# Kernel tuning notes

Hardware: AMD Instinct MI355X
Metric: run time of the kernel (lower is better)

Reference implementation:

```python
import jax, jax.numpy as jnp
import numpy as np

E, D, O, G, H, K = 8, 1024, 1024, 512, 2048, 2
B = 8192

def _xavier(key, shape):
    fan_in, fan_out = shape[-2], shape[-1]
    lim = float(np.sqrt(6.0 / (fan_in + fan_out)))
    return jax.random.uniform(key, shape, jnp.float32, -lim, lim)

def setup_inputs() -> dict:
    key = jax.random.key(0)
    ks = jax.random.split(key, 6)
    x = jax.random.normal(ks[0], (B, D), jnp.float32)
    # stacked expert params (xavier-uniform weights, zero bias like torch init)
    W1 = _xavier(ks[1], (E, D, H))
    b1 = jnp.zeros((E, H), jnp.float32)
    W2 = _xavier(ks[2], (E, H, O))
    b2 = jnp.zeros((E, O), jnp.float32)
    # gate params
    Wg1 = _xavier(ks[3], (D, G))
    bg1 = jnp.zeros((G,), jnp.float32)
    Wg2 = _xavier(ks[4], (G, E))
    bg2 = jnp.zeros((E,), jnp.float32)
    return {"x": x, "W1": W1, "b1": b1, "W2": W2, "b2": b2,
            "Wg1": Wg1, "bg1": bg1, "Wg2": Wg2, "bg2": bg2}

def reference(x, W1, b1, W2, b2, Wg1, bg1, Wg2, bg2):
    batch = x.shape[0]
    # gate (dropout inactive in eval)
    gate_logits = jax.nn.relu(x @ Wg1 + bg1) @ Wg2 + bg2          # [B,E]
    gate_scores = jax.nn.softmax(gate_logits, axis=1)
    top_k_scores, top_k_indices = jax.lax.top_k(gate_scores, K)   # [B,K]
    # dense all-expert MLP (mirrors torch.stack over experts)
    h = jax.nn.relu(jnp.einsum('bd,edh->ebh', x, W1) + b1[:, None, :])   # [E,B,H]
    expert_outputs = jnp.einsum('ebh,eho->beo', h, W2) + b2[None, :, :]  # [B,E,O]
    # gather top-k expert outputs, scale, combine
    selected = jnp.take_along_axis(expert_outputs, top_k_indices[:, :, None], axis=1)  # [B,K,O]
    scaled = selected * top_k_scores[:, :, None]
    scaled = scaled / (jnp.sum(top_k_scores, axis=1, keepdims=True)[:, :, None] + 1e-9)
    combined = jnp.sum(scaled, axis=1)                            # [B,O]
    # auxiliary loss
    one_hot = jax.nn.one_hot(top_k_indices, E, dtype=jnp.float32) # [B,K,E]
    expert_load = jnp.sum(one_hot, axis=(0, 1)) / (batch + 1e-9)
    load_balancing_loss = jnp.var(expert_load, ddof=1)            # torch var is unbiased
    entropy = -jnp.mean(jnp.sum(gate_scores * jnp.log(gate_scores + 1e-9), axis=1))
    aux_loss = load_balancing_loss + entropy
    return combined, aux_loss
```

## Files before the change

kernel.cpp:

```cpp
#include <hip/hip_runtime.h>

#define B_ 8192
#define D_ 1024
#define O_ 1024
#define G_ 512
#define H_ 2048
#define E_ 8
#define ROWSP (B_ * 2 + E_ * 128)
#define TAU 0.01f

typedef unsigned short u16;
using f32x4  = __attribute__((ext_vector_type(4))) float;
using s16x8  = __attribute__((ext_vector_type(8))) short;

__device__ __forceinline__ u16 f2bf(float f) {
  union { float f; unsigned u; } v; v.f = f;
  unsigned r = v.u + 0x7FFFu + ((v.u >> 16) & 1u);
  return (u16)(r >> 16);
}
__device__ __forceinline__ float bf2f(u16 h) {
  union { unsigned u; float f; } v; v.u = ((unsigned)h) << 16; return v.f;
}
__device__ __forceinline__ void gload16(const void* g, void* l) {
  __builtin_amdgcn_global_load_lds(
      (const __attribute__((address_space(1))) unsigned int*)g,
      (__attribute__((address_space(3))) unsigned int*)l, 16, 0, 0);
}
__device__ __forceinline__ int xcd_swz(int bid, int nwg) {
  return (bid & 7) * (nwg >> 3) + (bid >> 3);
}
__device__ __forceinline__ int stage_kc(int t) {
  return (((t & 3) ^ ((t >> 3) & 3)) * 8);
}
__device__ __forceinline__ int frag_idx(int lane, int i) {
  int row = i * 16 + (lane & 15);
  int s = (lane >> 4) ^ ((lane >> 1) & 3);
  return (row * 4 + s) * 8;
}

#define PREP_CAST_BLK (B_ * D_ / 4 / 256)
#define PREP_WG1_BLK  ((G_ / 32) * (D_ / 32))
#define PREP_W1_BLK   ((H_ / 32) * (D_ / 32) * E_)
#define PREP_W2_BLK   ((O_ / 32) * (H_ / 32) * E_)

__device__ __forceinline__ void tr_cast_tile(const float* __restrict__ src,
                                             u16* __restrict__ dhi,
                                             u16* __restrict__ dlo,
                                             int R, int C, int bx, int by,
                                             float (*tile)[33], int t) {
  int c0 = bx * 32, r0 = by * 32;
  {
    int row = t >> 3, col4 = (t & 7) * 4;
    float4 v = *(const float4*)(src + (size_t)(r0 + row) * C + c0 + col4);
    tile[row][col4] = v.x; tile[row][col4 + 1] = v.y;
    tile[row][col4 + 2] = v.z; tile[row][col4 + 3] = v.w;
  }
  __syncthreads();
  {
    int c = t >> 3, r4 = (t & 7) * 4;
    float v0 = tile[r4 + 0][c], v1 = tile[r4 + 1][c];
    float v2 = tile[r4 + 2][c], v3 = tile[r4 + 3][c];
    ushort4 hi;
    hi.x = f2bf(v0); hi.y = f2bf(v1); hi.z = f2bf(v2); hi.w = f2bf(v3);
    *(ushort4*)(dhi + (size_t)(c0 + c) * R + r0 + r4) = hi;
    if (dlo) {
      ushort4 lo;
      lo.x = f2bf(v0 - bf2f(hi.x)); lo.y = f2bf(v1 - bf2f(hi.y));
      lo.z = f2bf(v2 - bf2f(hi.z)); lo.w = f2bf(v3 - bf2f(hi.w));
      *(ushort4*)(dlo + (size_t)(c0 + c) * R + r0 + r4) = lo;
    }
  }
}

__global__ __launch_bounds__(256) void k_prep(const float* __restrict__ x,
                                              u16* __restrict__ xhi, u16* __restrict__ xlo,
                                              const float* __restrict__ Wg1,
                                              u16* __restrict__ wg1h, u16* __restrict__ wg1l,
                                              const float* __restrict__ W1, u16* __restrict__ w1t,
                                              const float* __restrict__ W2, u16* __restrict__ w2t) {
  __shared__ float tile[32][33];
  int t = threadIdx.x;
  int b = blockIdx.x;
  if (b < PREP_CAST_BLK) {
    int i = b * 256 + t;
    float4 v = ((const float4*)x)[i];
    u16 h0 = f2bf(v.x), h1 = f2bf(v.y), h2 = f2bf(v.z), h3 = f2bf(v.w);
    ushort4 hi; hi.x = h0; hi.y = h1; hi.z = h2; hi.w = h3;
    ushort4 lo;
    lo.x = f2bf(v.x - bf2f(h0)); lo.y = f2bf(v.y - bf2f(h1));
    lo.z = f2bf(v.z - bf2f(h2)); lo.w = f2bf(v.w - bf2f(h3));
    ((ushort4*)xhi)[i] = hi; ((ushort4*)xlo)[i] = lo;
    return;
  }
  b -= PREP_CAST_BLK;
  if (b < PREP_WG1_BLK) {
    tr_cast_tile(Wg1, wg1h, wg1l, D_, G_, b & 15, b >> 4, tile, t);
    return;
  }
  b -= PREP_WG1_BLK;
  if (b < PREP_W1_BLK) {
    int e = b >> 11, rr = b & 2047;
    size_t ofs = (size_t)e * D_ * H_;
    tr_cast_tile(W1 + ofs, w1t + ofs, nullptr, D_, H_, rr & 63, rr >> 6, tile, t);
    return;
  }
  b -= PREP_W1_BLK;
  {
    int e = b >> 11, rr = b & 2047;
    size_t ofs = (size_t)e * H_ * O_;
    tr_cast_tile(W2 + ofs, w2t + ofs, nullptr, H_, O_, rr & 31, rr >> 5, tile, t);
  }
}

__global__ __launch_bounds__(256) void k_gate_gemm1(const u16* __restrict__ xhi,
                                                    const u16* __restrict__ xlo,
                                                    const u16* __restrict__ whi,
                                                    const u16* __restrict__ wlo,
                                                    const float* __restrict__ bg1,
                                                    float* __restrict__ G1) {
  __shared__ u16 Ah[2048], Al[2048], Bh[4096], Bl[4096];
  int work = xcd_swz(blockIdx.x, (G_ / 128) * (B_ / 64));
  int m0 = (work >> 2) * 64, n0 = (work & 3) * 128;
  int t = threadIdx.x;
  int wave = t >> 6, lane = t & 63;
  int wm = wave >> 1, wn = wave & 1;

  const f32x4 z = {0.f, 0.f, 0.f, 0.f};
  f32x4 acc[2][4];
#pragma unroll
  for (int i = 0; i < 2; ++i)
#pragma unroll
    for (int j = 0; j < 4; ++j) acc[i][j] = z;

  int ar = t >> 2, ac = stage_kc(t);
  const u16* xh0 = xhi + (size_t)(m0 + ar) * D_ + ac;
  const u16* xl0 = xlo + (size_t)(m0 + ar) * D_ + ac;
  const u16* wh0 = whi + (size_t)(n0 + ar) * D_ + ac;
  const u16* wh1 = whi + (size_t)(n0 + 64 + ar) * D_ + ac;
  const u16* wl0 = wlo + (size_t)(n0 + ar) * D_ + ac;
  const u16* wl1 = wlo + (size_t)(n0 + 64 + ar) * D_ + ac;

  for (int k0 = 0; k0 < D_; k0 += 32) {
    gload16(xh0 + k0, &Ah[t * 8]);
    gload16(xl0 + k0, &Al[t * 8]);
    gload16(wh0 + k0, &Bh[t * 8]); gload16(wh1 + k0, &Bh[2048 + t * 8]);
    gload16(wl0 + k0, &Bl[t * 8]); gload16(wl1 + k0, &Bl[2048 + t * 8]);
    __syncthreads();
    s16x8 ah[2], al[2], bh[4], bl[4];
#pragma unroll
    for (int i = 0; i < 2; ++i) {
      ah[i] = *(const s16x8*)&Ah[frag_idx(lane, wm * 2 + i)];
      al[i] = *(const s16x8*)&Al[frag_idx(lane, wm * 2 + i)];
    }
#pragma unroll
    for (int j = 0; j < 4; ++j) {
      bh[j] = *(const s16x8*)&Bh[wn * 2048 + frag_idx(lane, j)];
      bl[j] = *(const s16x8*)&Bl[wn * 2048 + frag_idx(lane, j)];
    }
#pragma unroll
    for (int i = 0; i < 2; ++i)
#pragma unroll
      for (int j = 0; j < 4; ++j) {
        acc[i][j] = __builtin_amdgcn_mfma_f32_16x16x32_bf16(ah[i], bh[j], acc[i][j], 0, 0, 0);
        acc[i][j] = __builtin_amdgcn_mfma_f32_16x16x32_bf16(ah[i], bl[j], acc[i][j], 0, 0, 0);
        acc[i][j] = __builtin_amdgcn_mfma_f32_16x16x32_bf16(al[i], bh[j], acc[i][j], 0, 0, 0);
      }
    __syncthreads();
  }
#pragma unroll
  for (int j = 0; j < 4; ++j) {
    int col = n0 + wn * 64 + j * 16 + (lane & 15);
    float bias = bg1[col];
#pragma unroll
    for (int i = 0; i < 2; ++i)
#pragma unroll
      for (int q = 0; q < 4; ++q) {
        int row = m0 + wm * 32 + i * 16 + (lane >> 4) * 4 + q;
        float v = acc[i][j][q] + bias;
        G1[(size_t)row * G_ + col] = v > 0.f ? v : 0.f;
      }
  }
}

__global__ __launch_bounds__(256) void k_gate_logits(const float* __restrict__ G1,
                                                     const float* __restrict__ Wg2,
                                                     const float* __restrict__ bg2,
                                                     float* __restrict__ logits,
                                                     int* __restrict__ flaglist,
                                                     int* __restrict__ nflag) {
  int t = threadIdx.x, wave = t >> 6, lane = t & 63;
  int row = blockIdx.x * 4 + wave;

  float4 g0 = *(const float4*)(G1 + (size_t)row * G_ + lane * 8);
  float4 g1 = *(const float4*)(G1 + (size_t)row * G_ + lane * 8 + 4);
  float g[8] = {g0.x, g0.y, g0.z, g0.w, g1.x, g1.y, g1.z, g1.w};
  float p[8] = {0, 0, 0, 0, 0, 0, 0, 0};
#pragma unroll
  for (int cc = 0; cc < 8; ++cc) {
    int c = lane * 8 + cc;
    float4 w0 = *(const float4*)(Wg2 + c * 8);
    float4 w1 = *(const float4*)(Wg2 + c * 8 + 4);
    p[0] += g[cc] * w0.x; p[1] += g[cc] * w0.y; p[2] += g[cc] * w0.z; p[3] += g[cc] * w0.w;
    p[4] += g[cc] * w1.x; p[5] += g[cc] * w1.y; p[6] += g[cc] * w1.z; p[7] += g[cc] * w1.w;
  }
#pragma unroll
  for (int off = 32; off >= 1; off >>= 1)
#pragma unroll
    for (int e = 0; e < 8; ++e) p[e] += __shfl_xor(p[e], off);
  if (lane == 0) {
    float l1 = -1e30f, l2 = -1e30f, l3 = -1e30f;
#pragma unroll
    for (int e = 0; e < 8; ++e) {
      float v = p[e] + bg2[e];
      logits[(size_t)row * 8 + e] = v;
      if (v > l1) { l3 = l2; l2 = l1; l1 = v; }
      else if (v > l2) { l3 = l2; l2 = v; }
      else if (v > l3) { l3 = v; }
    }
    if (l2 - l3 < TAU) {
      int pos = atomicAdd(nflag, 1);
      flaglist[pos] = row;
    }
  }
}

__global__ __launch_bounds__(256) void k_gate_fixup(const float* __restrict__ x,
                                                    const float* __restrict__ Wg1,
                                                    const float* __restrict__ bg1,
                                                    const float* __restrict__ Wg2,
                                                    const float* __restrict__ bg2,
                                                    const int* __restrict__ flaglist,
                                                    const int* __restrict__ nflag,
                                                    float* __restrict__ logits) {
  __shared__ float xs[1024];
  __shared__ float red[256][9];
  int t = threadIdx.x;
  int n = *nflag;
  for (int i = blockIdx.x; i < n; i += gridDim.x) {
    int row = flaglist[i];
    ((float4*)xs)[t] = ((const float4*)(x + (size_t)row * D_))[t];
    __syncthreads();
    int c0 = t * 2;
    float h0 = 0.f, h1 = 0.f;
#pragma unroll 8
    for (int d = 0; d < D_; ++d) {
      float xv = xs[d];
      float2 w = *(const float2*)(Wg1 + (size_t)d * G_ + c0);
      h0 += xv * w.x; h1 += xv * w.y;
    }
    h0 += bg1[c0]; h1 += bg1[c0 + 1];
    h0 = h0 > 0.f ? h0 : 0.f; h1 = h1 > 0.f ? h1 : 0.f;
#pragma unroll
    for (int e = 0; e < 8; ++e)
      red[t][e] = h0 * Wg2[c0 * 8 + e] + h1 * Wg2[(c0 + 1) * 8 + e];
    __syncthreads();
    for (int s = 128; s >= 1; s >>= 1) {
      if (t < s) {
#pragma unroll
        for (int e = 0; e < 8; ++e) red[t][e] += red[t + s][e];
      }
      __syncthreads();
    }
    if (t < 8) logits[(size_t)row * 8 + t] = red[0][t] + bg2[t];
    __syncthreads();
  }
}

__global__ __launch_bounds__(256) void k_gate_final(const float* __restrict__ logits,
                                                    int* __restrict__ topidx,
                                                    float* __restrict__ wnorm,
                                                    int* __restrict__ counts,
                                                    float* __restrict__ entacc) {
  __shared__ int cnt_s[8];
  __shared__ float ent_s[4];
  int t = threadIdx.x;
  if (t < 8) cnt_s[t] = 0;
  __syncthreads();
  int row = blockIdx.x * 256 + t;
  float4 a = ((const float4*)logits)[(size_t)row * 2];
  float4 b = ((const float4*)logits)[(size_t)row * 2 + 1];
  float L[8] = {a.x, a.y, a.z, a.w, b.x, b.y, b.z, b.w};
  float m = L[0];
#pragma unroll
  for (int e = 1; e < 8; ++e) m = fmaxf(m, L[e]);
  float s[8], Z = 0.f;
#pragma unroll
  for (int e = 0; e < 8; ++e) { s[e] = expf(L[e] - m); Z += s[e]; }
  float inv = 1.f / Z;
  float sc[8];
#pragma unroll
  for (int e = 0; e < 8; ++e) sc[e] = s[e] * inv;
  int i1 = 0;
#pragma unroll
  for (int e = 1; e < 8; ++e) if (L[e] > L[i1]) i1 = e;
  int i2 = (i1 == 0) ? 1 : 0;
#pragma unroll
  for (int e = 0; e < 8; ++e) if (e != i1 && L[e] > L[i2]) i2 = e;
  float s1 = sc[i1], s2 = sc[i2];
  float denom = s1 + s2 + 1e-9f;
  topidx[row * 2] = i1; topidx[row * 2 + 1] = i2;
  wnorm[row * 2] = s1 / denom; wnorm[row * 2 + 1] = s2 / denom;
  atomicAdd(&cnt_s[i1], 1); atomicAdd(&cnt_s[i2], 1);
  float ent = 0.f;
#pragma unroll
  for (int e = 0; e < 8; ++e) ent -= sc[e] * logf(sc[e] + 1e-9f);
#pragma unroll
  for (int off = 32; off >= 1; off >>= 1) ent += __shfl_xor(ent, off);
  if ((t & 63) == 0) ent_s[t >> 6] = ent;
  __syncthreads();
  if (t == 0) atomicAdd(entacc, ent_s[0] + ent_s[1] + ent_s[2] + ent_s[3]);
  if (t < 8) atomicAdd(&counts[t], cnt_s[t]);
}

__global__ void k_scan(const int* __restrict__ counts, const float* __restrict__ entacc,
                       int* __restrict__ aoff, float* __restrict__ aux_out) {
  if (threadIdx.x == 0 && blockIdx.x == 0) {
    int off = 0; aoff[0] = 0;
    float ld[8]; float mean = 0.f;
    for (int e = 0; e < 8; ++e) {
      ld[e] = (float)counts[e] / (8192.0f + 1e-9f);
      mean += ld[e];
      off += ((counts[e] + 127) >> 7) << 7;
      aoff[e + 1] = off;
    }
    mean *= 0.125f;
    float var = 0.f;
    for (int e = 0; e < 8; ++e) { float d = ld[e] - mean; var += d * d; }
    var *= (1.0f / 7.0f);
    *aux_out = var + entacc[0] / 8192.0f;
  }
}

__global__ __launch_bounds__(256) void k_scatter(const int* __restrict__ topidx,
                                                 const float* __restrict__ wnorm,
                                                 const int* __restrict__ aoff,
                                                 int* __restrict__ fill,
                                                 int* __restrict__ tok_list,
                                                 float* __restrict__ wroute,
                                                 int* __restrict__ pos_of) {
  int t = blockIdx.x * 256 + threadIdx.x;
  if (t >= B_ * 2) return;
  int e = topidx[t];
  int pos = aoff[e] + atomicAdd(&fill[e], 1);
  tok_list[pos] = t >> 1;
  wroute[pos] = wnorm[t];
  pos_of[t] = pos;
}


__global__ __launch_bounds__(256) void k_egemm1(const u16* __restrict__ xhi,
                                                const u16* __restrict__ w1t,
                                                const float* __restrict__ b1v,
                                                const int* __restrict__ tok_list,
                                                const int* __restrict__ aoff,
                                                u16* __restrict__ hbuf) {
  __shared__ u16 As[2][4096], Bs[2][4096];
  int work = xcd_swz(blockIdx.x, (H_ / 128) * (ROWSP / 128));
  int rt = work >> 4;
  int n0 = (work & 15) * 128;
  int row0 = rt * 128;
  if (row0 >= aoff[8]) return;
  int e = 0;
  while (row0 >= aoff[e + 1]) ++e;
  int t = threadIdx.x, wave = t >> 6, lane = t & 63;
  int wm = wave >> 1, wn = wave & 1;
  const u16* w1e = w1t + (size_t)e * H_ * D_;

  int ar = t >> 2, ac = stage_kc(t);
  int tok0 = tok_list[row0 + ar];       if ((unsigned)tok0 >= B_) tok0 = 0;
  int tok1 = tok_list[row0 + 64 + ar];  if ((unsigned)tok1 >= B_) tok1 = 0;
  const u16* a0 = xhi + (size_t)tok0 * D_ + ac;
  const u16* a1 = xhi + (size_t)tok1 * D_ + ac;
  const u16* bb0 = w1e + (size_t)(n0 + ar) * D_ + ac;
  const u16* bb1 = w1e + (size_t)(n0 + 64 + ar) * D_ + ac;

  const f32x4 z = {0.f, 0.f, 0.f, 0.f};
  f32x4 acc[4][4];
#pragma unroll
  for (int i = 0; i < 4; ++i)
#pragma unroll
    for (int j = 0; j < 4; ++j) acc[i][j] = z;

  gload16(a0, &As[0][t * 8]);  gload16(a1, &As[0][2048 + t * 8]);
  gload16(bb0, &Bs[0][t * 8]); gload16(bb1, &Bs[0][2048 + t * 8]);
  __syncthreads();

  const int NT = D_ / 32;
  for (int kt = 0; kt < NT; ++kt) {
    int cur = kt & 1, nxt = cur ^ 1;
    if (kt + 1 < NT) {
      int kk = (kt + 1) * 32;
      gload16(a0 + kk, &As[nxt][t * 8]);  gload16(a1 + kk, &As[nxt][2048 + t * 8]);
      gload16(bb0 + kk, &Bs[nxt][t * 8]); gload16(bb1 + kk, &Bs[nxt][2048 + t * 8]);
    }
    s16x8 af[4], bf[4];
#pragma unroll
    for (int i = 0; i < 4; ++i) {
      af[i] = *(const s16x8*)&As[cur][wm * 2048 + frag_idx(lane, i)];
      bf[i] = *(const s16x8*)&Bs[cur][wn * 2048 + frag_idx(lane, i)];
    }
#pragma unroll
    for (int i = 0; i < 4; ++i)
#pragma unroll
      for (int j = 0; j < 4; ++j)
        acc[i][j] = __builtin_amdgcn_mfma_f32_16x16x32_bf16(af[i], bf[j], acc[i][j], 0, 0, 0);
    __syncthreads();
  }
#pragma unroll
  for (int j = 0; j < 4; ++j) {
    int col = n0 + wn * 64 + j * 16 + (lane & 15);
    float bias = b1v[e * H_ + col];
#pragma unroll
    for (int i = 0; i < 4; ++i)
#pragma unroll
      for (int q = 0; q < 4; ++q) {
        int row = row0 + wm * 64 + i * 16 + (lane >> 4) * 4 + q;
        float v = acc[i][j][q] + bias;
        hbuf[(size_t)row * H_ + col] = f2bf(v > 0.f ? v : 0.f);
      }
  }
}

__global__ __launch_bounds__(256) void k_egemm2(const u16* __restrict__ hbuf,
                                                const u16* __restrict__ w2t,
                                                const float* __restrict__ b2v,
                                                const int* __restrict__ aoff,
                                                const float* __restrict__ wroute,
                                                u16* __restrict__ rbuf) {
  __shared__ u16 As[2][4096], Bs[2][4096];
  int work = xcd_swz(blockIdx.x, (O_ / 128) * (ROWSP / 128));
  int rt = work >> 3;
  int n0 = (work & 7) * 128;
  int row0 = rt * 128;
  if (row0 >= aoff[8]) return;
  int e = 0;
  while (row0 >= aoff[e + 1]) ++e;
  int t = threadIdx.x, wave = t >> 6, lane = t & 63;
  int wm = wave >> 1, wn = wave & 1;
  const u16* w2e = w2t + (size_t)e * O_ * H_;

  int ar = t >> 2, ac = stage_kc(t);
  const u16* a0 = hbuf + (size_t)(row0 + ar) * H_ + ac;
  const u16* a1 = hbuf + (size_t)(row0 + 64 + ar) * H_ + ac;
  const u16* bb0 = w2e + (size_t)(n0 + ar) * H_ + ac;
  const u16* bb1 = w2e + (size_t)(n0 + 64 + ar) * H_ + ac;

  const f32x4 z = {0.f, 0.f, 0.f, 0.f};
  f32x4 acc[4][4];
#pragma unroll
  for (int i = 0; i < 4; ++i)
#pragma unroll
    for (int j = 0; j < 4; ++j) acc[i][j] = z;

  gload16(a0, &As[0][t * 8]);  gload16(a1, &As[0][2048 + t * 8]);
  gload16(bb0, &Bs[0][t * 8]); gload16(bb1, &Bs[0][2048 + t * 8]);
  __syncthreads();

  const int NT = H_ / 32;
  for (int kt = 0; kt < NT; ++kt) {
    int cur = kt & 1, nxt = cur ^ 1;
    if (kt + 1 < NT) {
      int kk = (kt + 1) * 32;
      gload16(a0 + kk, &As[nxt][t * 8]);  gload16(a1 + kk, &As[nxt][2048 + t * 8]);
      gload16(bb0 + kk, &Bs[nxt][t * 8]); gload16(bb1 + kk, &Bs[nxt][2048 + t * 8]);
    }
    s16x8 af[4], bf[4];
#pragma unroll
    for (int i = 0; i < 4; ++i) {
      af[i] = *(const s16x8*)&As[cur][wm * 2048 + frag_idx(lane, i)];
      bf[i] = *(const s16x8*)&Bs[cur][wn * 2048 + frag_idx(lane, i)];
    }
#pragma unroll
    for (int i = 0; i < 4; ++i)
#pragma unroll
      for (int j = 0; j < 4; ++j)
        acc[i][j] = __builtin_amdgcn_mfma_f32_16x16x32_bf16(af[i], bf[j], acc[i][j], 0, 0, 0);
    __syncthreads();
  }
#pragma unroll
  for (int i = 0; i < 4; ++i)
#pragma unroll
    for (int q = 0; q < 4; ++q) {
      int row = row0 + wm * 64 + i * 16 + (lane >> 4) * 4 + q;
      float wv = wroute[row];
#pragma unroll
      for (int j = 0; j < 4; ++j) {
        int col = n0 + wn * 64 + j * 16 + (lane & 15);
        float bias = b2v[e * O_ + col];
        rbuf[(size_t)row * O_ + col] = f2bf((acc[i][j][q] + bias) * wv);
      }
    }
}

__global__ __launch_bounds__(256) void k_combine(const u16* __restrict__ rbuf,
                                                 const int* __restrict__ pos_of,
                                                 float* __restrict__ out) {
  int t = threadIdx.x;
  int tok = blockIdx.x * 2 + (t >> 7);
  int c = (t & 127) * 8;
  int p0 = pos_of[tok * 2], p1 = pos_of[tok * 2 + 1];
  const u16* r0 = rbuf + (size_t)p0 * O_ + c;
  const u16* r1 = rbuf + (size_t)p1 * O_ + c;
  ushort4 a0 = *(const ushort4*)r0, a1 = *(const ushort4*)(r0 + 4);
  ushort4 b0 = *(const ushort4*)r1, b1 = *(const ushort4*)(r1 + 4);
  float4 o0, o1;
  o0.x = bf2f(a0.x) + bf2f(b0.x); o0.y = bf2f(a0.y) + bf2f(b0.y);
  o0.z = bf2f(a0.z) + bf2f(b0.z); o0.w = bf2f(a0.w) + bf2f(b0.w);
  o1.x = bf2f(a1.x) + bf2f(b1.x); o1.y = bf2f(a1.y) + bf2f(b1.y);
  o1.z = bf2f(a1.z) + bf2f(b1.z); o1.w = bf2f(a1.w) + bf2f(b1.w);
  float* op = out + (size_t)tok * O_ + c;
  *(float4*)op = o0; *(float4*)(op + 4) = o1;
}

static const size_t o_xhi  = 0;
static const size_t o_xlo  = o_xhi + (size_t)B_ * D_ * 2;
static const size_t o_w1t  = o_xlo + (size_t)B_ * D_ * 2;
static const size_t o_w2t  = o_w1t + (size_t)E_ * H_ * D_ * 2;
static const size_t o_wg1h = o_w2t + (size_t)E_ * O_ * H_ * 2;
static const size_t o_wg1l = o_wg1h + (size_t)G_ * D_ * 2;
static const size_t o_G1   = o_wg1l + (size_t)G_ * D_ * 2;
static const size_t o_h    = o_G1 + (size_t)B_ * G_ * 4;
static const size_t o_idx  = o_h + (size_t)ROWSP * H_ * 2;
static const size_t o_wn   = o_idx + (size_t)B_ * 2 * 4;
static const size_t o_pos  = o_wn + (size_t)B_ * 2 * 4;
static const size_t o_tok  = o_pos + (size_t)B_ * 2 * 4;
static const size_t o_wr   = o_tok + (size_t)ROWSP * 4;
static const size_t o_cnt  = o_wr + (size_t)ROWSP * 4;
static const size_t o_fill = o_cnt + 32;
static const size_t o_ent  = o_cnt + 64;
static const size_t o_nfl  = o_cnt + 96;
static const size_t o_aoff = o_cnt + 128;
static const size_t o_logits = o_cnt + 256;
static const size_t o_flag   = o_logits + (size_t)B_ * 8 * 4;
static const size_t o_rbuf = o_xlo;

extern "C" void kernel_launch(void* const* d_in, const int* in_sizes, int n_in,
                              void* d_out, int out_size, void* d_ws, size_t ws_size,
                              hipStream_t stream) {
  const float* x   = (const float*)d_in[0];
  const float* W1  = (const float*)d_in[1];
  const float* b1  = (const float*)d_in[2];
  const float* W2  = (const float*)d_in[3];
  const float* b2  = (const float*)d_in[4];
  const float* Wg1 = (const float*)d_in[5];
  const float* bg1 = (const float*)d_in[6];
  const float* Wg2 = (const float*)d_in[7];
  const float* bg2 = (const float*)d_in[8];
  float* out = (float*)d_out;
  char* ws = (char*)d_ws;

  u16* xhi  = (u16*)(ws + o_xhi);
  u16* xlo  = (u16*)(ws + o_xlo);
  u16* w1t  = (u16*)(ws + o_w1t);
  u16* w2t  = (u16*)(ws + o_w2t);
  u16* wg1h = (u16*)(ws + o_wg1h);
  u16* wg1l = (u16*)(ws + o_wg1l);
  float* G1 = (float*)(ws + o_G1);
  u16* hbuf = (u16*)(ws + o_h);
  int* topidx = (int*)(ws + o_idx);
  float* wnorm = (float*)(ws + o_wn);
  int* pos_of = (int*)(ws + o_pos);
  int* tok_list = (int*)(ws + o_tok);
  float* wroute = (float*)(ws + o_wr);
  int* counts = (int*)(ws + o_cnt);
  int* fill = (int*)(ws + o_fill);
  float* entacc = (float*)(ws + o_ent);
  int* nflag = (int*)(ws + o_nfl);
  int* aoff = (int*)(ws + o_aoff);
  float* logits = (float*)(ws + o_logits);
  int* flaglist = (int*)(ws + o_flag);
  u16* rbuf = (u16*)(ws + o_rbuf);

  hipMemsetAsync(ws + o_cnt, 0, 128, stream);

  k_prep<<<PREP_CAST_BLK + PREP_WG1_BLK + PREP_W1_BLK + PREP_W2_BLK, 256, 0, stream>>>(
      x, xhi, xlo, Wg1, wg1h, wg1l, W1, w1t, W2, w2t);

  k_gate_gemm1<<<(G_ / 128) * (B_ / 64), 256, 0, stream>>>(xhi, xlo, wg1h, wg1l, bg1, G1);
  k_gate_logits<<<B_ / 4, 256, 0, stream>>>(G1, Wg2, bg2, logits, flaglist, nflag);
  k_gate_fixup<<<128, 256, 0, stream>>>(x, Wg1, bg1, Wg2, bg2, flaglist, nflag, logits);
  k_gate_final<<<B_ / 256, 256, 0, stream>>>(logits, topidx, wnorm, counts, entacc);
  k_scan<<<1, 64, 0, stream>>>(counts, entacc, aoff, out + (size_t)B_ * O_);
  k_scatter<<<(B_ * 2) / 256, 256, 0, stream>>>(topidx, wnorm, aoff, fill, tok_list, wroute, pos_of);

  k_egemm1<<<(H_ / 128) * (ROWSP / 128), 256, 0, stream>>>(xhi, w1t, b1, tok_list, aoff, hbuf);
  k_egemm2<<<(O_ / 128) * (ROWSP / 128), 256, 0, stream>>>(hbuf, w2t, b2, aoff, wroute, rbuf);
  k_combine<<<B_ / 2, 256, 0, stream>>>(rbuf, pos_of, out);
}
```

Before: 496.9 us.

## Fuse gate fixup, scan and scatter into gate kernels; drop x low-part split

Removes the low bf16 residual of x, so the gate GEMM does two MFMAs per tile instead of three and the prep kernel writes half as much x data. To make up for the lost precision, TAU is raised so more rows with close second and third logits are recomputed in fp32. That recomputation now runs inside k_gate_logits, per block, instead of in a separate fixup kernel. k_scan and k_scatter are folded into k_gate_final through a grid-wide spin barrier on an arrival counter, and the memset is replaced by zeroing inside k_prep. The spin barrier assumes all 32 blocks of k_gate_final are resident at once, and the in-block fixup can serialize blocks that hold flagged rows.

```diff
diff --git a/kernel.cpp b/kernel.cpp
--- a/kernel.cpp
+++ b/kernel.cpp
@@ -7,7 +7,7 @@
 #define H_ 2048
 #define E_ 8
 #define ROWSP (B_ * 2 + E_ * 128)
-#define TAU 0.01f
+#define TAU 0.04f
 
 typedef unsigned short u16;
 using f32x4  = __attribute__((ext_vector_type(4))) float;
@@ -73,23 +73,22 @@
 }
 
 __global__ __launch_bounds__(256) void k_prep(const float* __restrict__ x,
-                                              u16* __restrict__ xhi, u16* __restrict__ xlo,
+                                              u16* __restrict__ xhi,
                                               const float* __restrict__ Wg1,
                                               u16* __restrict__ wg1h, u16* __restrict__ wg1l,
                                               const float* __restrict__ W1, u16* __restrict__ w1t,
-                                              const float* __restrict__ W2, u16* __restrict__ w2t) {
+                                              const float* __restrict__ W2, u16* __restrict__ w2t,
+                                              int* __restrict__ zeroarea) {
   __shared__ float tile[32][33];
   int t = threadIdx.x;
   int b = blockIdx.x;
   if (b < PREP_CAST_BLK) {
+    if (b == 0 && t < 32) zeroarea[t] = 0;
     int i = b * 256 + t;
     float4 v = ((const float4*)x)[i];
-    u16 h0 = f2bf(v.x), h1 = f2bf(v.y), h2 = f2bf(v.z), h3 = f2bf(v.w);
-    ushort4 hi; hi.x = h0; hi.y = h1; hi.z = h2; hi.w = h3;
-    ushort4 lo;
-    lo.x = f2bf(v.x - bf2f(h0)); lo.y = f2bf(v.y - bf2f(h1));
-    lo.z = f2bf(v.z - bf2f(h2)); lo.w = f2bf(v.w - bf2f(h3));
-    ((ushort4*)xhi)[i] = hi; ((ushort4*)xlo)[i] = lo;
+    ushort4 hi;
+    hi.x = f2bf(v.x); hi.y = f2bf(v.y); hi.z = f2bf(v.z); hi.w = f2bf(v.w);
+    ((ushort4*)xhi)[i] = hi;
     return;
   }
   b -= PREP_CAST_BLK;
@@ -113,12 +112,11 @@
 }
 
 __global__ __launch_bounds__(256) void k_gate_gemm1(const u16* __restrict__ xhi,
-                                                    const u16* __restrict__ xlo,
                                                     const u16* __restrict__ whi,
                                                     const u16* __restrict__ wlo,
                                                     const float* __restrict__ bg1,
                                                     float* __restrict__ G1) {
-  __shared__ u16 Ah[2048], Al[2048], Bh[4096], Bl[4096];
+  __shared__ u16 Ah[2048], Bh[4096], Bl[4096];
   int work = xcd_swz(blockIdx.x, (G_ / 128) * (B_ / 64));
   int m0 = (work >> 2) * 64, n0 = (work & 3) * 128;
   int t = threadIdx.x;
@@ -134,7 +132,6 @@
 
   int ar = t >> 2, ac = stage_kc(t);
   const u16* xh0 = xhi + (size_t)(m0 + ar) * D_ + ac;
-  const u16* xl0 = xlo + (size_t)(m0 + ar) * D_ + ac;
   const u16* wh0 = whi + (size_t)(n0 + ar) * D_ + ac;
   const u16* wh1 = whi + (size_t)(n0 + 64 + ar) * D_ + ac;
   const u16* wl0 = wlo + (size_t)(n0 + ar) * D_ + ac;
@@ -142,16 +139,13 @@
 
   for (int k0 = 0; k0 < D_; k0 += 32) {
     gload16(xh0 + k0, &Ah[t * 8]);
-    gload16(xl0 + k0, &Al[t * 8]);
     gload16(wh0 + k0, &Bh[t * 8]); gload16(wh1 + k0, &Bh[2048 + t * 8]);
     gload16(wl0 + k0, &Bl[t * 8]); gload16(wl1 + k0, &Bl[2048 + t * 8]);
     __syncthreads();
-    s16x8 ah[2], al[2], bh[4], bl[4];
-#pragma unroll
-    for (int i = 0; i < 2; ++i) {
+    s16x8 ah[2], bh[4], bl[4];
+#pragma unroll
+    for (int i = 0; i < 2; ++i)
       ah[i] = *(const s16x8*)&Ah[frag_idx(lane, wm * 2 + i)];
-      al[i] = *(const s16x8*)&Al[frag_idx(lane, wm * 2 + i)];
-    }
 #pragma unroll
     for (int j = 0; j < 4; ++j) {
       bh[j] = *(const s16x8*)&Bh[wn * 2048 + frag_idx(lane, j)];
@@ -163,7 +157,6 @@
       for (int j = 0; j < 4; ++j) {
         acc[i][j] = __builtin_amdgcn_mfma_f32_16x16x32_bf16(ah[i], bh[j], acc[i][j], 0, 0, 0);
         acc[i][j] = __builtin_amdgcn_mfma_f32_16x16x32_bf16(ah[i], bl[j], acc[i][j], 0, 0, 0);
-        acc[i][j] = __builtin_amdgcn_mfma_f32_16x16x32_bf16(al[i], bh[j], acc[i][j], 0, 0, 0);
       }
     __syncthreads();
   }
@@ -183,11 +176,15 @@
 }
 
 __global__ __launch_bounds__(256) void k_gate_logits(const float* __restrict__ G1,
+                                                     const float* __restrict__ x,
+                                                     const float* __restrict__ Wg1,
+                                                     const float* __restrict__ bg1,
                                                      const float* __restrict__ Wg2,
                                                      const float* __restrict__ bg2,
-                                                     float* __restrict__ logits,
-                                                     int* __restrict__ flaglist,
-                                                     int* __restrict__ nflag) {
+                                                     float* __restrict__ logits) {
+  __shared__ int flagsm[4];
+  __shared__ float xs[1024];
+  __shared__ float red[256][9];
   int t = threadIdx.x, wave = t >> 6, lane = t & 63;
   int row = blockIdx.x * 4 + wave;
 
@@ -217,52 +214,38 @@
       else if (v > l2) { l3 = l2; l2 = v; }
       else if (v > l3) { l3 = v; }
     }
-    if (l2 - l3 < TAU) {
-      int pos = atomicAdd(nflag, 1);
-      flaglist[pos] = row;
-    }
-  }
-}
-
-__global__ __launch_bounds__(256) void k_gate_fixup(const float* __restrict__ x,
-                                                    const float* __restrict__ Wg1,
-                                                    const float* __restrict__ bg1,
-                                                    const float* __restrict__ Wg2,
-                                                    const float* __restrict__ bg2,
-                                                    const int* __restrict__ flaglist,
-                                                    const int* __restrict__ nflag,
-                                                    float* __restrict__ logits) {
-  __shared__ float xs[1024];
-  __shared__ float red[256][9];
-  int t = threadIdx.x;
-  int n = *nflag;
-  for (int i = blockIdx.x; i < n; i += gridDim.x) {
-    int row = flaglist[i];
-    ((float4*)xs)[t] = ((const float4*)(x + (size_t)row * D_))[t];
-    __syncthreads();
-    int c0 = t * 2;
-    float h0 = 0.f, h1 = 0.f;
+    flagsm[wave] = (l2 - l3 < TAU) ? 1 : 0;
+  }
+  __syncthreads();
+  for (int r = 0; r < 4; ++r) {
+    if (flagsm[r]) {
+      int rr = blockIdx.x * 4 + r;
+      ((float4*)xs)[t] = ((const float4*)(x + (size_t)rr * D_))[t];
+      __syncthreads();
+      int c0 = t * 2;
+      float h0 = 0.f, h1 = 0.f;
 #pragma unroll 8
-    for (int d = 0; d < D_; ++d) {
-      float xv = xs[d];
-      float2 w = *(const float2*)(Wg1 + (size_t)d * G_ + c0);
-      h0 += xv * w.x; h1 += xv * w.y;
-    }
-    h0 += bg1[c0]; h1 += bg1[c0 + 1];
-    h0 = h0 > 0.f ? h0 : 0.f; h1 = h1 > 0.f ? h1 : 0.f;
-#pragma unroll
-    for (int e = 0; e < 8; ++e)
-      red[t][e] = h0 * Wg2[c0 * 8 + e] + h1 * Wg2[(c0 + 1) * 8 + e];
-    __syncthreads();
-    for (int s = 128; s >= 1; s >>= 1) {
-      if (t < s) {
-#pragma unroll
-        for (int e = 0; e < 8; ++e) red[t][e] += red[t + s][e];
+      for (int d = 0; d < D_; ++d) {
+        float xv = xs[d];
+        float2 w = *(const float2*)(Wg1 + (size_t)d * G_ + c0);
+        h0 += xv * w.x; h1 += xv * w.y;
       }
+      h0 += bg1[c0]; h1 += bg1[c0 + 1];
+      h0 = h0 > 0.f ? h0 : 0.f; h1 = h1 > 0.f ? h1 : 0.f;
+#pragma unroll
+      for (int e = 0; e < 8; ++e)
+        red[t][e] = h0 * Wg2[c0 * 8 + e] + h1 * Wg2[(c0 + 1) * 8 + e];
       __syncthreads();
-    }
-    if (t < 8) logits[(size_t)row * 8 + t] = red[0][t] + bg2[t];
-    __syncthreads();
+      for (int s = 128; s >= 1; s >>= 1) {
+        if (t < s) {
+#pragma unroll
+          for (int e = 0; e < 8; ++e) red[t][e] += red[t + s][e];
+        }
+        __syncthreads();
+      }
+      if (t < 8) logits[(size_t)rr * 8 + t] = red[0][t] + bg2[t];
+      __syncthreads();
+    }
   }
 }
 
@@ -270,9 +253,17 @@
                                                     int* __restrict__ topidx,
                                                     float* __restrict__ wnorm,
                                                     int* __restrict__ counts,
-                                                    float* __restrict__ entacc) {
+                                                    float* __restrict__ entacc,
+                                                    int* __restrict__ arrive,
+                                                    int* __restrict__ fill,
+                                                    int* __restrict__ tok_list,
+                                                    float* __restrict__ wroute,
+                                                    int* __restrict__ pos_of,
+                                                    int* __restrict__ aoff,
+                                                    float* __restrict__ aux_out) {
   __shared__ int cnt_s[8];
   __shared__ float ent_s[4];
+  __shared__ int aoff_s[9];
   int t = threadIdx.x;
   if (t < 8) cnt_s[t] = 0;
   __syncthreads();
@@ -298,8 +289,9 @@
   for (int e = 0; e < 8; ++e) if (e != i1 && L[e] > L[i2]) i2 = e;
   float s1 = sc[i1], s2 = sc[i2];
   float denom = s1 + s2 + 1e-9f;
+  float w1v = s1 / denom, w2v = s2 / denom;
   topidx[row * 2] = i1; topidx[row * 2 + 1] = i2;
-  wnorm[row * 2] = s1 / denom; wnorm[row * 2 + 1] = s2 / denom;
+  wnorm[row * 2] = w1v; wnorm[row * 2 + 1] = w2v;
   atomicAdd(&cnt_s[i1], 1); atomicAdd(&cnt_s[i2], 1);
   float ent = 0.f;
 #pragma unroll
@@ -310,41 +302,39 @@
   __syncthreads();
   if (t == 0) atomicAdd(entacc, ent_s[0] + ent_s[1] + ent_s[2] + ent_s[3]);
   if (t < 8) atomicAdd(&counts[t], cnt_s[t]);
-}
-
-__global__ void k_scan(const int* __restrict__ counts, const float* __restrict__ entacc,
-                       int* __restrict__ aoff, float* __restrict__ aux_out) {
-  if (threadIdx.x == 0 && blockIdx.x == 0) {
-    int off = 0; aoff[0] = 0;
-    float ld[8]; float mean = 0.f;
+  __threadfence();
+  __syncthreads();
+  if (t == 0) {
+    atomicAdd(arrive, 1);
+    while (atomicAdd(arrive, 0) < (int)gridDim.x) { }
+    int off = 0; aoff_s[0] = 0;
+    int cn[8];
     for (int e = 0; e < 8; ++e) {
-      ld[e] = (float)counts[e] / (8192.0f + 1e-9f);
-      mean += ld[e];
-      off += ((counts[e] + 127) >> 7) << 7;
-      aoff[e + 1] = off;
-    }
-    mean *= 0.125f;
-    float var = 0.f;
-    for (int e = 0; e < 8; ++e) { float d = ld[e] - mean; var += d * d; }
-    var *= (1.0f / 7.0f);
-    *aux_out = var + entacc[0] / 8192.0f;
-  }
-}
-
-__global__ __launch_bounds__(256) void k_scatter(const int* __restrict__ topidx,
-                                                 const float* __restrict__ wnorm,
-                                                 const int* __restrict__ aoff,
-                                                 int* __restrict__ fill,
-                                                 int* __restrict__ tok_list,
-                                                 float* __restrict__ wroute,
-                                                 int* __restrict__ pos_of) {
-  int t = blockIdx.x * 256 + threadIdx.x;
-  if (t >= B_ * 2) return;
-  int e = topidx[t];
-  int pos = aoff[e] + atomicAdd(&fill[e], 1);
-  tok_list[pos] = t >> 1;
-  wroute[pos] = wnorm[t];
-  pos_of[t] = pos;
+      cn[e] = atomicAdd(&counts[e], 0);
+      off += ((cn[e] + 127) >> 7) << 7;
+      aoff_s[e + 1] = off;
+    }
+    if (blockIdx.x == 0) {
+      for (int e = 0; e < 9; ++e) aoff[e] = aoff_s[e];
+      float mean = 0.f, ld[8];
+      for (int e = 0; e < 8; ++e) { ld[e] = (float)cn[e] / (8192.0f + 1e-9f); mean += ld[e]; }
+      mean *= 0.125f;
+      float var = 0.f;
+      for (int e = 0; e < 8; ++e) { float d = ld[e] - mean; var += d * d; }
+      var *= (1.0f / 7.0f);
+      float entv = atomicAdd(entacc, 0.f);
+      *aux_out = var + entv / 8192.0f;
+    }
+  }
+  __syncthreads();
+  {
+    int pos = aoff_s[i1] + atomicAdd(&fill[i1], 1);
+    tok_list[pos] = row; wroute[pos] = w1v; pos_of[row * 2] = pos;
+  }
+  {
+    int pos = aoff_s[i2] + atomicAdd(&fill[i2], 1);
+    tok_list[pos] = row; wroute[pos] = w2v; pos_of[row * 2 + 1] = pos;
+  }
 }
 
 
@@ -528,10 +518,9 @@
 static const size_t o_cnt  = o_wr + (size_t)ROWSP * 4;
 static const size_t o_fill = o_cnt + 32;
 static const size_t o_ent  = o_cnt + 64;
-static const size_t o_nfl  = o_cnt + 96;
+static const size_t o_arr  = o_cnt + 96;
 static const size_t o_aoff = o_cnt + 128;
 static const size_t o_logits = o_cnt + 256;
-static const size_t o_flag   = o_logits + (size_t)B_ * 8 * 4;
 static const size_t o_rbuf = o_xlo;
 
 extern "C" void kernel_launch(void* const* d_in, const int* in_sizes, int n_in,
@@ -550,7 +539,6 @@
   char* ws = (char*)d_ws;
 
   u16* xhi  = (u16*)(ws + o_xhi);
-  u16* xlo  = (u16*)(ws + o_xlo);
   u16* w1t  = (u16*)(ws + o_w1t);
   u16* w2t  = (u16*)(ws + o_w2t);
   u16* wg1h = (u16*)(ws + o_wg1h);
@@ -565,23 +553,19 @@
   int* counts = (int*)(ws + o_cnt);
   int* fill = (int*)(ws + o_fill);
   float* entacc = (float*)(ws + o_ent);
-  int* nflag = (int*)(ws + o_nfl);
+  int* arrive = (int*)(ws + o_arr);
   int* aoff = (int*)(ws + o_aoff);
   float* logits = (float*)(ws + o_logits);
-  int* flaglist = (int*)(ws + o_flag);
   u16* rbuf = (u16*)(ws + o_rbuf);
 
-  hipMemsetAsync(ws + o_cnt, 0, 128, stream);
-
   k_prep<<<PREP_CAST_BLK + PREP_WG1_BLK + PREP_W1_BLK + PREP_W2_BLK, 256, 0, stream>>>(
-      x, xhi, xlo, Wg1, wg1h, wg1l, W1, w1t, W2, w2t);
-
-  k_gate_gemm1<<<(G_ / 128) * (B_ / 64), 256, 0, stream>>>(xhi, xlo, wg1h, wg1l, bg1, G1);
-  k_gate_logits<<<B_ / 4, 256, 0, stream>>>(G1, Wg2, bg2, logits, flaglist, nflag);
-  k_gate_fixup<<<128, 256, 0, stream>>>(x, Wg1, bg1, Wg2, bg2, flaglist, nflag, logits);
-  k_gate_final<<<B_ / 256, 256, 0, stream>>>(logits, topidx, wnorm, counts, entacc);
-  k_scan<<<1, 64, 0, stream>>>(counts, entacc, aoff, out + (size_t)B_ * O_);
-  k_scatter<<<(B_ * 2) / 256, 256, 0, stream>>>(topidx, wnorm, aoff, fill, tok_list, wroute, pos_of);
+      x, xhi, Wg1, wg1h, wg1l, W1, w1t, W2, w2t, counts);
+
+  k_gate_gemm1<<<(G_ / 128) * (B_ / 64), 256, 0, stream>>>(xhi, wg1h, wg1l, bg1, G1);
+  k_gate_logits<<<B_ / 4, 256, 0, stream>>>(G1, x, Wg1, bg1, Wg2, bg2, logits);
+  k_gate_final<<<B_ / 256, 256, 0, stream>>>(logits, topidx, wnorm, counts, entacc, arrive,
+                                             fill, tok_list, wroute, pos_of, aoff,
+                                             out + (size_t)B_ * O_);
 
   k_egemm1<<<(H_ / 128) * (ROWSP / 128), 256, 0, stream>>>(xhi, w1t, b1, tok_list, aoff, hbuf);
   k_egemm2<<<(O_ / 128) * (ROWSP / 128), 256, 0, stream>>>(hbuf, w2t, b2, aoff, wroute, rbuf);
```

New measurement: 603.0 us. 21.3% more time.
